# Optimization experiments

Measured on AMD Instinct MI355X. Metric: run time of the kernel, lower is better.

The kernel has to match this reference:

```python
import jax, jax.numpy as jnp
import numpy as np

N_HEADS = 16


def sparsemax(z):
    """Sparsemax along the last axis (Martins & Astudillo 2016)."""
    S = z.shape[-1]
    z_sorted = -jnp.sort(-z, axis=-1)                      # descending
    cs = jnp.cumsum(z_sorted, axis=-1)
    k = jnp.arange(1, S + 1, dtype=z.dtype)
    support = (1.0 + k * z_sorted) > cs                    # bool mask of support
    k_z = jnp.sum(support.astype(jnp.int32), axis=-1, keepdims=True)  # support size >=1
    cs_k = jnp.take_along_axis(cs, k_z - 1, axis=-1)
    tau = (cs_k - 1.0) / k_z.astype(z.dtype)
    return jnp.maximum(z - tau, 0.0)


def setup_inputs() -> dict:
    key = jax.random.key(0)
    ks = jax.random.split(key, 5)
    B, S, D = 4, 1024, 1024
    scale = 1.0 / np.sqrt(D).astype(np.float32)
    return {
        "x": jax.random.normal(ks[0], (B, S, D), jnp.float32),
        "Wq": jax.random.normal(ks[1], (D, D), jnp.float32) * scale,
        "bq": jnp.zeros((D,), jnp.float32),
        "Wk": jax.random.normal(ks[2], (D, D), jnp.float32) * scale,
        "bk": jnp.zeros((D,), jnp.float32),
        "Wv": jax.random.normal(ks[3], (D, D), jnp.float32) * scale,
        "bv": jnp.zeros((D,), jnp.float32),
        "Wo": jax.random.normal(ks[4], (D, D), jnp.float32) * scale,
        "bo": jnp.zeros((D,), jnp.float32),
    }


def reference(x, Wq, bq, Wk, bk, Wv, bv, Wo, bo):
    B, S, D = x.shape
    H = N_HEADS
    dh = D // H
    q = x @ Wq + bq                                        # (B,S,D)
    k = x @ Wk + bk
    v = x @ Wv + bv
    # split to heads: (B,H,S,dh)
    qh = q.reshape(B, S, H, dh).transpose(0, 2, 1, 3)
    kh = k.reshape(B, S, H, dh).transpose(0, 2, 1, 3)
    logits = jnp.einsum("bhqd,bhkd->bhqk", qh, kh) / np.sqrt(dh).astype(np.float32)
    probs = sparsemax(logits)                              # (B,H,S,S)
    # shared V: mean over head components, replicated per head
    v_shared = v.reshape(B, S, H, dh).mean(axis=2)         # (B,S,dh)
    out_h = jnp.einsum("bhqk,bkd->bhqd", probs, v_shared)  # (B,H,S,dh)
    x_out = out_h.transpose(0, 2, 1, 3).reshape(B, S, D) @ Wo + bo
    avg_attention = probs.mean(axis=1)                     # (B,S,S)
    return (x_out, avg_attention)
```

## Files before the change

kernel.cpp:

```cpp
#include <hip/hip_runtime.h>

#define B_  4
#define S_  1024
#define D_  1024
#define H_  16
#define DH  64
#define BS  4096

typedef __bf16 bf16x8 __attribute__((ext_vector_type(8)));
typedef float  f32x4  __attribute__((ext_vector_type(4)));

__device__ __forceinline__ unsigned short f2bf(float f) {
    __bf16 b = (__bf16)f;
    return __builtin_bit_cast(unsigned short, b);
}
__device__ __forceinline__ float bf2f(unsigned short u) {
    return (float)__builtin_bit_cast(__bf16, u);
}
__device__ __forceinline__ void glds16(const void* g, void* l) {
    __builtin_amdgcn_global_load_lds((const __attribute__((address_space(1))) void*)g,
                                     (__attribute__((address_space(3))) void*)l, 16, 0, 0);
}

__global__ __launch_bounds__(256) void prep2(const float* __restrict__ Wq,
                                             const float* __restrict__ Wk,
                                             const float* __restrict__ Wo,
                                             const float* __restrict__ Wv,
                                             const float* __restrict__ bv,
                                             unsigned short* __restrict__ WqTh,
                                             unsigned short* __restrict__ WqTl,
                                             unsigned short* __restrict__ WkTh,
                                             unsigned short* __restrict__ WkTl,
                                             unsigned short* __restrict__ WoTh,
                                             unsigned short* __restrict__ WvTh,
                                             unsigned short* __restrict__ WvTl,
                                             float* __restrict__ bvp) {
    __shared__ float tile[32][33];
    int bid = blockIdx.x, tid = threadIdx.x;
    if (bid < 3072) {
        const float* W;
        unsigned short *Th, *Tl;
        int wantLo;
        if (bid < 1024)      { W = Wq; Th = WqTh; Tl = WqTl; wantLo = 1; }
        else if (bid < 2048) { W = Wk; Th = WkTh; Tl = WkTl; wantLo = 1; bid -= 1024; }
        else                 { W = Wo; Th = WoTh; Tl = nullptr; wantLo = 0; bid -= 2048; }
        int tn = bid & 31, tk = bid >> 5;
        int r = tid >> 3, c4 = (tid & 7) * 4;
        float4 v = *(const float4*)(W + (size_t)(tk * 32 + r) * D_ + tn * 32 + c4);
        tile[r][c4 + 0] = v.x;
        tile[r][c4 + 1] = v.y;
        tile[r][c4 + 2] = v.z;
        tile[r][c4 + 3] = v.w;
        __syncthreads();
        unsigned short hh[4], ll[4];
#pragma unroll
        for (int i = 0; i < 4; i++) {
            float f = tile[c4 + i][r];
            hh[i] = f2bf(f);
            ll[i] = f2bf(f - bf2f(hh[i]));
        }
        size_t off = (size_t)(tn * 32 + r) * D_ + tk * 32 + c4;
        *(uint2*)(Th + off) = make_uint2((unsigned)hh[0] | ((unsigned)hh[1] << 16),
                                         (unsigned)hh[2] | ((unsigned)hh[3] << 16));
        if (wantLo)
            *(uint2*)(Tl + off) = make_uint2((unsigned)ll[0] | ((unsigned)ll[1] << 16),
                                             (unsigned)ll[2] | ((unsigned)ll[3] << 16));
    } else if (bid < 3328) {
        int e = (bid - 3072) * 256 + tid;
        int d = e >> 6, j = e & 63;
        float s = 0.f;
#pragma unroll
        for (int hh = 0; hh < H_; hh++) s += Wv[(size_t)d * D_ + hh * DH + j];
        s *= (1.f / 16.f);
        unsigned short hi = f2bf(s);
        WvTh[(size_t)j * D_ + d] = hi;
        WvTl[(size_t)j * D_ + d] = f2bf(s - bf2f(hi));
        if (bid == 3072 && tid < 128) {
            float sb = 0.f;
            if (tid < 64) {
#pragma unroll
                for (int hh = 0; hh < H_; hh++) sb += bv[hh * DH + tid];
                sb *= (1.f / 16.f);
            }
            bvp[tid] = sb;
        }
    } else {
        int e = (bid - 3328) * 256 + tid;
        int row = 64 + (e >> 10), col = e & 1023;
        WvTh[(size_t)row * D_ + col] = 0;
        WvTl[(size_t)row * D_ + col] = 0;
    }
}

__global__ __launch_bounds__(256) void projg(const float* __restrict__ x,
                                             const unsigned short* __restrict__ WqTh, const unsigned short* __restrict__ WqTl,
                                             const unsigned short* __restrict__ WkTh, const unsigned short* __restrict__ WkTl,
                                             const unsigned short* __restrict__ WvTh, const unsigned short* __restrict__ WvTl,
                                             const float* __restrict__ bq, const float* __restrict__ bk,
                                             const float* __restrict__ bvp,
                                             unsigned short* __restrict__ qh, unsigned short* __restrict__ ql,
                                             unsigned short* __restrict__ kh, unsigned short* __restrict__ kl,
                                             float* __restrict__ vshb) {
    __shared__ unsigned short AhS[128 * 32];
    __shared__ unsigned short AlS[128 * 32];
    __shared__ unsigned short BhS[128 * 32];
    __shared__ unsigned short BlS[128 * 32];

    int tid = threadIdx.x, w = tid >> 6, lane = tid & 63;
    int m16 = lane & 15, qd = lane >> 4;
    int bn = blockIdx.x, bm = blockIdx.y;

    const unsigned short *Bh, *Bl;
    const float* bias;
    int mode;
    if (bn < 8)       { Bh = WqTh + (size_t)bn * 128 * D_;       Bl = WqTl + (size_t)bn * 128 * D_;       bias = bq + bn * 128;       mode = 0; }
    else if (bn < 16) { Bh = WkTh + (size_t)(bn - 8) * 128 * D_; Bl = WkTl + (size_t)(bn - 8) * 128 * D_; bias = bk + (bn - 8) * 128; mode = 1; }
    else              { Bh = WvTh; Bl = WvTl; bias = bvp; mode = 2; }

    int l4 = lane >> 2, c8 = (lane & 3) * 8;
    int rh = (w >> 1) * 64, chh = (w & 1) * 64;

    f32x4 acc[4][4];
#pragma unroll
    for (int it = 0; it < 4; it++)
#pragma unroll
        for (int jt = 0; jt < 4; jt++) acc[it][jt] = (f32x4){0.f, 0.f, 0.f, 0.f};

    int ra = tid >> 1, ca = (tid & 1) * 16;

    for (int k0 = 0; k0 < D_; k0 += 32) {
        const float* ax = x + (size_t)(bm * 128 + ra) * D_ + k0 + ca;
        float4 f0 = *(const float4*)(ax + 0);
        float4 f1 = *(const float4*)(ax + 4);
        float4 f2 = *(const float4*)(ax + 8);
        float4 f3 = *(const float4*)(ax + 12);
        __syncthreads();
        {
            float vv[16] = {f0.x, f0.y, f0.z, f0.w, f1.x, f1.y, f1.z, f1.w,
                            f2.x, f2.y, f2.z, f2.w, f3.x, f3.y, f3.z, f3.w};
            unsigned int hw[8], lw[8];
#pragma unroll
            for (int i = 0; i < 8; i++) {
                unsigned short h0 = f2bf(vv[2 * i]), h1 = f2bf(vv[2 * i + 1]);
                unsigned short l0 = f2bf(vv[2 * i] - bf2f(h0));
                unsigned short l1 = f2bf(vv[2 * i + 1] - bf2f(h1));
                hw[i] = (unsigned)h0 | ((unsigned)h1 << 16);
                lw[i] = (unsigned)l0 | ((unsigned)l1 << 16);
            }
            char* ah = (char*)AhS + ra * 64 + ca * 2;
            char* al = (char*)AlS + ra * 64 + ca * 2;
            *(uint4*)(ah + 0)  = make_uint4(hw[0], hw[1], hw[2], hw[3]);
            *(uint4*)(ah + 16) = make_uint4(hw[4], hw[5], hw[6], hw[7]);
            *(uint4*)(al + 0)  = make_uint4(lw[0], lw[1], lw[2], lw[3]);
            *(uint4*)(al + 16) = make_uint4(lw[4], lw[5], lw[6], lw[7]);
        }
        {
            const unsigned short* gbh = Bh + (size_t)(w * 32 + l4) * D_ + k0 + c8;
            const unsigned short* gbl = Bl + (size_t)(w * 32 + l4) * D_ + k0 + c8;
            glds16(gbh,                     (char*)BhS + w * 2048);
            glds16(gbh + (size_t)16 * D_,   (char*)BhS + w * 2048 + 1024);
            glds16(gbl,                     (char*)BlS + w * 2048);
            glds16(gbl + (size_t)16 * D_,   (char*)BlS + w * 2048 + 1024);
        }
        __syncthreads();
        bf16x8 ah[4], al[4], bh[4], bl[4];
#pragma unroll
        for (int it = 0; it < 4; it++) {
            ah[it] = *(const bf16x8*)((char*)AhS + (rh + it * 16 + m16) * 64 + qd * 16);
            al[it] = *(const bf16x8*)((char*)AlS + (rh + it * 16 + m16) * 64 + qd * 16);
        }
#pragma unroll
        for (int jt = 0; jt < 4; jt++) {
            bh[jt] = *(const bf16x8*)((char*)BhS + (chh + jt * 16 + m16) * 64 + qd * 16);
            bl[jt] = *(const bf16x8*)((char*)BlS + (chh + jt * 16 + m16) * 64 + qd * 16);
        }
#pragma unroll
        for (int it = 0; it < 4; it++)
#pragma unroll
            for (int jt = 0; jt < 4; jt++) {
                acc[it][jt] = __builtin_amdgcn_mfma_f32_16x16x32_bf16(ah[it], bh[jt], acc[it][jt], 0, 0, 0);
                acc[it][jt] = __builtin_amdgcn_mfma_f32_16x16x32_bf16(ah[it], bl[jt], acc[it][jt], 0, 0, 0);
                acc[it][jt] = __builtin_amdgcn_mfma_f32_16x16x32_bf16(al[it], bh[jt], acc[it][jt], 0, 0, 0);
            }
    }
#pragma unroll
    for (int it = 0; it < 4; it++)
#pragma unroll
        for (int jt = 0; jt < 4; jt++)
#pragma unroll
            for (int r = 0; r < 4; r++) {
                int R = bm * 128 + rh + it * 16 + qd * 4 + r;
                int c = chh + jt * 16 + m16;
                float v = acc[it][jt][r] + bias[c];
                if (mode == 0) {
                    v *= 0.125f;
                    unsigned short h0 = f2bf(v);
                    qh[(size_t)R * D_ + bn * 128 + c] = h0;
                    ql[(size_t)R * D_ + bn * 128 + c] = f2bf(v - bf2f(h0));
                } else if (mode == 1) {
                    unsigned short h0 = f2bf(v);
                    kh[(size_t)R * D_ + (bn - 8) * 128 + c] = h0;
                    kl[(size_t)R * D_ + (bn - 8) * 128 + c] = f2bf(v - bf2f(h0));
                } else {
                    if (c < 64) vshb[(size_t)R * 64 + c] = v;
                }
            }
}

__global__ __launch_bounds__(256) void outg(const unsigned short* __restrict__ A,
                                            const unsigned short* __restrict__ Bh,
                                            const float* __restrict__ bias,
                                            float* __restrict__ C) {
    __shared__ unsigned short AhS[128 * 32];
    __shared__ unsigned short BhS[128 * 32];

    int tid = threadIdx.x, w = tid >> 6, lane = tid & 63;
    int m16 = lane & 15, qd = lane >> 4;
    int bn = blockIdx.x, bm = blockIdx.y;
    int l4 = lane >> 2, c8 = (lane & 3) * 8;
    int rh = (w >> 1) * 64, chh = (w & 1) * 64;

    f32x4 acc[4][4];
#pragma unroll
    for (int it = 0; it < 4; it++)
#pragma unroll
        for (int jt = 0; jt < 4; jt++) acc[it][jt] = (f32x4){0.f, 0.f, 0.f, 0.f};

    for (int k0 = 0; k0 < D_; k0 += 32) {
        __syncthreads();
        {
            const unsigned short* ga = A + (size_t)(bm * 128 + w * 32 + l4) * D_ + k0 + c8;
            glds16(ga,                   (char*)AhS + w * 2048);
            glds16(ga + (size_t)16 * D_, (char*)AhS + w * 2048 + 1024);
            const unsigned short* gb = Bh + (size_t)(bn * 128 + w * 32 + l4) * D_ + k0 + c8;
            glds16(gb,                   (char*)BhS + w * 2048);
            glds16(gb + (size_t)16 * D_, (char*)BhS + w * 2048 + 1024);
        }
        __syncthreads();
        bf16x8 ah[4], bh[4];
#pragma unroll
        for (int it = 0; it < 4; it++)
            ah[it] = *(const bf16x8*)((char*)AhS + (rh + it * 16 + m16) * 64 + qd * 16);
#pragma unroll
        for (int jt = 0; jt < 4; jt++)
            bh[jt] = *(const bf16x8*)((char*)BhS + (chh + jt * 16 + m16) * 64 + qd * 16);
#pragma unroll
        for (int it = 0; it < 4; it++)
#pragma unroll
            for (int jt = 0; jt < 4; jt++)
                acc[it][jt] = __builtin_amdgcn_mfma_f32_16x16x32_bf16(ah[it], bh[jt], acc[it][jt], 0, 0, 0);
    }
#pragma unroll
    for (int it = 0; it < 4; it++)
#pragma unroll
        for (int jt = 0; jt < 4; jt++)
#pragma unroll
            for (int r = 0; r < 4; r++) {
                int R = bm * 128 + rh + it * 16 + qd * 4 + r;
                int cc = bn * 128 + chh + jt * 16 + m16;
                C[(size_t)R * D_ + cc] = acc[it][jt][r] + bias[cc];
            }
}

#define CCAP 48
__global__ __launch_bounds__(256, 2) void attn8(const unsigned short* __restrict__ qh,
                                                const unsigned short* __restrict__ ql,
                                                const unsigned short* __restrict__ kh,
                                                const unsigned short* __restrict__ kl,
                                                const float* __restrict__ vsh,
                                                unsigned short* __restrict__ och,
                                                unsigned short* __restrict__ sidx,
                                                unsigned short* __restrict__ sval,
                                                int* __restrict__ scnt) {
    __shared__ float smM[4][16];
    __shared__ float smS[4][16], smC[4][16];
    __shared__ float tau0s[16];
    __shared__ float taus[16];
    __shared__ float candV[16][CCAP];
    __shared__ short candI[16][CCAP];
    __shared__ int   ccnt[16];
    __shared__ int   ovfAny;
    __shared__ int   scnt16[16];
    __shared__ short slotI[16][16];
    __shared__ float slotV[16][16];

    int tid = threadIdx.x, w = tid >> 6, lane = tid & 63;
    int m16 = lane & 15, qd = lane >> 4;

    int bid = blockIdx.x;
    int xcd = bid & 7;
    int j   = bid >> 3;
    int bh  = ((j & 7) << 3) | xcd;
    int qt  = j >> 3;
    int bb  = bh >> 4, h = bh & 15;
    int row0g = bb * S_ + qt * 16;
    int kbase = bb * S_;

    bf16x8 aH[2], aL[2];
#pragma unroll
    for (int c = 0; c < 2; c++) {
        size_t off = (size_t)(row0g + m16) * D_ + h * DH + c * 32 + qd * 8;
        aH[c] = *(const bf16x8*)(qh + off);
        aL[c] = *(const bf16x8*)(ql + off);
    }

    f32x4 Cfr[16];
#pragma unroll
    for (int t = 0; t < 16; t++) Cfr[t] = (f32x4){0.f, 0.f, 0.f, 0.f};

#pragma unroll
    for (int tb = 0; tb < 4; tb++) {
        bf16x8 bH[4][2], bL[4][2];
#pragma unroll
        for (int tt = 0; tt < 4; tt++) {
            int n0 = w * 256 + (tb * 4 + tt) * 16;
#pragma unroll
            for (int c = 0; c < 2; c++) {
                size_t boff = (size_t)(kbase + n0 + m16) * D_ + h * DH + c * 32 + qd * 8;
                bH[tt][c] = *(const bf16x8*)(kh + boff);
                bL[tt][c] = *(const bf16x8*)(kl + boff);
            }
        }
#pragma unroll
        for (int tt = 0; tt < 4; tt++) {
            int t = tb * 4 + tt;
            f32x4 a = Cfr[t];
            a = __builtin_amdgcn_mfma_f32_16x16x32_bf16(aH[0], bH[tt][0], a, 0, 0, 0);
            a = __builtin_amdgcn_mfma_f32_16x16x32_bf16(aH[1], bH[tt][1], a, 0, 0, 0);
            a = __builtin_amdgcn_mfma_f32_16x16x32_bf16(aH[0], bL[tt][0], a, 0, 0, 0);
            a = __builtin_amdgcn_mfma_f32_16x16x32_bf16(aH[1], bL[tt][1], a, 0, 0, 0);
            a = __builtin_amdgcn_mfma_f32_16x16x32_bf16(aL[0], bH[tt][0], a, 0, 0, 0);
            a = __builtin_amdgcn_mfma_f32_16x16x32_bf16(aL[1], bH[tt][1], a, 0, 0, 0);
            Cfr[t] = a;
        }
    }

    float mxr[4];
#pragma unroll
    for (int r = 0; r < 4; r++) mxr[r] = -3.0e38f;
#pragma unroll
    for (int t = 0; t < 16; t++)
#pragma unroll
        for (int r = 0; r < 4; r++) mxr[r] = fmaxf(mxr[r], Cfr[t][r]);
#pragma unroll
    for (int off = 8; off >= 1; off >>= 1)
#pragma unroll
        for (int r = 0; r < 4; r++) mxr[r] = fmaxf(mxr[r], __shfl_xor(mxr[r], off, 16));
    if (m16 == 0)
#pragma unroll
        for (int r = 0; r < 4; r++) smM[w][qd * 4 + r] = mxr[r];
    if (tid < 16) ccnt[tid] = 0;
    if (tid == 0) ovfAny = 0;
    __syncthreads();
    if (tid < 16)
        tau0s[tid] = fmaxf(fmaxf(smM[0][tid], smM[1][tid]), fmaxf(smM[2][tid], smM[3][tid])) - 1.0f;
    __syncthreads();

#pragma unroll
    for (int t = 0; t < 16; t++)
#pragma unroll
        for (int r = 0; r < 4; r++) {
            float z = Cfr[t][r];
            int row = qd * 4 + r;
            if (z > tau0s[row]) {
                int pos = atomicAdd(&ccnt[row], 1);
                if (pos < CCAP) {
                    candV[row][pos] = z;
                    candI[row][pos] = (short)(w * 256 + t * 16 + m16);
                }
            }
        }
    __syncthreads();
    if (tid < 16 && ccnt[tid] > CCAP) ovfAny = 1;

    int prow = tid >> 4, pc = tid & 15;
    int nc = ccnt[prow];
    float tau = tau0s[prow];
    float z0 = -3.0e38f, z1 = -3.0e38f, z2 = -3.0e38f;
    if (nc <= CCAP) {
        z0 = (pc < nc)      ? candV[prow][pc]      : -3.0e38f;
        z1 = (pc + 16 < nc) ? candV[prow][pc + 16] : -3.0e38f;
        z2 = (pc + 32 < nc) ? candV[prow][pc + 32] : -3.0e38f;
        for (int it = 0; it < CCAP; it++) {
            float s = 0.f, c = 0.f;
            if (z0 > tau) { s += z0; c += 1.f; }
            if (z1 > tau) { s += z1; c += 1.f; }
            if (z2 > tau) { s += z2; c += 1.f; }
#pragma unroll
            for (int off = 8; off >= 1; off >>= 1) {
                s += __shfl_xor(s, off, 16);
                c += __shfl_xor(c, off, 16);
            }
            float tnew = (s - 1.f) / c;
            if (tnew > tau) tau = tnew; else break;
        }
    }
    if (pc == 0) taus[prow] = tau;
    if (tid < 16) scnt16[tid] = 0;
    __syncthreads();

    if (!ovfAny) {
        if (z0 > tau) {
            int sl = atomicAdd(&scnt16[prow], 1);
            if (sl < 16) { slotI[prow][sl] = candI[prow][pc]; slotV[prow][sl] = z0 - tau; }
        }
        if (z1 > tau) {
            int sl = atomicAdd(&scnt16[prow], 1);
            if (sl < 16) { slotI[prow][sl] = candI[prow][pc + 16]; slotV[prow][sl] = z1 - tau; }
        }
        if (z2 > tau) {
            int sl = atomicAdd(&scnt16[prow], 1);
            if (sl < 16) { slotI[prow][sl] = candI[prow][pc + 32]; slotV[prow][sl] = z2 - tau; }
        }
        __syncthreads();
    } else {
        for (int it = 0; it < 64; it++) {
            float s[4], c[4];
#pragma unroll
            for (int r = 0; r < 4; r++) { s[r] = 0.f; c[r] = 0.f; }
#pragma unroll
            for (int t = 0; t < 16; t++)
#pragma unroll
                for (int r = 0; r < 4; r++) {
                    float z = Cfr[t][r];
                    if (z > taus[qd * 4 + r]) { s[r] += z; c[r] += 1.f; }
                }
#pragma unroll
            for (int off = 8; off >= 1; off >>= 1)
#pragma unroll
                for (int r = 0; r < 4; r++) {
                    s[r] += __shfl_xor(s[r], off, 16);
                    c[r] += __shfl_xor(c[r], off, 16);
                }
            if (m16 == 0)
#pragma unroll
                for (int r = 0; r < 4; r++) {
                    smS[w][qd * 4 + r] = s[r];
                    smC[w][qd * 4 + r] = c[r];
                }
            __syncthreads();
            int done = 1;
            if (tid < 16) {
                float S = smS[0][tid] + smS[1][tid] + smS[2][tid] + smS[3][tid];
                float C = smC[0][tid] + smC[1][tid] + smC[2][tid] + smC[3][tid];
                float tnew = (S - 1.f) / C;
                if (C > 0.f && tnew > taus[tid]) { taus[tid] = tnew; done = 0; }
            }
            if (__syncthreads_and(done)) break;
        }
#pragma unroll
        for (int t = 0; t < 16; t++)
#pragma unroll
            for (int r = 0; r < 4; r++) {
                int row = qd * 4 + r;
                float p = Cfr[t][r] - taus[row];
                if (p > 0.f) {
                    int sl = atomicAdd(&scnt16[row], 1);
                    if (sl < 16) {
                        slotI[row][sl] = (short)(w * 256 + t * 16 + m16);
                        slotV[row][sl] = p;
                    }
                }
            }
        __syncthreads();
    }

    int nsl = min(scnt16[prow], 16);
    float4 accq = make_float4(0.f, 0.f, 0.f, 0.f);
    for (int sl = 0; sl < nsl; sl++) {
        int key = slotI[prow][sl];
        float p = slotV[prow][sl];
        float4 vv = *(const float4*)(vsh + (size_t)(kbase + key) * DH + pc * 4);
        accq.x += p * vv.x;
        accq.y += p * vv.y;
        accq.z += p * vv.z;
        accq.w += p * vv.w;
    }
    {
        unsigned short b0 = f2bf(accq.x), b1 = f2bf(accq.y), b2 = f2bf(accq.z), b3 = f2bf(accq.w);
        *(uint2*)(och + (size_t)(row0g + prow) * D_ + h * DH + pc * 4) =
            make_uint2((unsigned)b0 | ((unsigned)b1 << 16), (unsigned)b2 | ((unsigned)b3 << 16));
    }
    {
        size_t base = ((size_t)(row0g + prow) * H_ + h) * 16;
        if (pc == 0) scnt[(row0g + prow) * H_ + h] = nsl;
        if (pc < nsl) {
            sidx[base + pc] = (unsigned short)slotI[prow][pc];
            sval[base + pc] = f2bf(slotV[prow][pc]);
        }
    }
}

__global__ __launch_bounds__(256) void avg_reduce(const unsigned short* __restrict__ sidx,
                                                  const unsigned short* __restrict__ sval,
                                                  const int* __restrict__ scnt,
                                                  float* __restrict__ avg) {
    __shared__ float accv[1024];
    int tid = threadIdx.x;
    int grow = blockIdx.x;
    for (int i = tid; i < 1024; i += 256) accv[i] = 0.f;
    __syncthreads();
    int h = tid >> 4, sl = tid & 15;
    int n = scnt[grow * H_ + h];
    if (sl < n) {
        size_t base = ((size_t)grow * H_ + h) * 16;
        int idx = sidx[base + sl];
        float v = bf2f(sval[base + sl]);
        atomicAdd(&accv[idx], v);
    }
    __syncthreads();
    float* dst = avg + (size_t)grow * S_;
    for (int i = tid; i < 256; i += 256) {
        float4 o;
        o.x = accv[i * 4 + 0] * 0.0625f;
        o.y = accv[i * 4 + 1] * 0.0625f;
        o.z = accv[i * 4 + 2] * 0.0625f;
        o.w = accv[i * 4 + 3] * 0.0625f;
        *(float4*)(dst + i * 4) = o;
    }
}

extern "C" void kernel_launch(void* const* d_in, const int* in_sizes, int n_in,
                              void* d_out, int out_size, void* d_ws, size_t ws_size,
                              hipStream_t stream) {
    const float* x  = (const float*)d_in[0];
    const float* Wq = (const float*)d_in[1];
    const float* bq = (const float*)d_in[2];
    const float* Wk = (const float*)d_in[3];
    const float* bk = (const float*)d_in[4];
    const float* Wv = (const float*)d_in[5];
    const float* bv = (const float*)d_in[6];
    const float* Wo = (const float*)d_in[7];
    const float* bo = (const float*)d_in[8];

    float* xout = (float*)d_out;
    float* avg  = xout + (size_t)BS * D_;

    char* ws = (char*)d_ws;
    unsigned short* qhB  = (unsigned short*)(ws + 0);
    unsigned short* qlB  = (unsigned short*)(ws + (8u << 20));
    unsigned short* khB  = (unsigned short*)(ws + (16u << 20));
    unsigned short* klB  = (unsigned short*)(ws + (24u << 20));
    unsigned short* WqTh = (unsigned short*)(ws + (32u << 20));
    unsigned short* WqTl = (unsigned short*)(ws + (34u << 20));
    unsigned short* WkTh = (unsigned short*)(ws + (36u << 20));
    unsigned short* WkTl = (unsigned short*)(ws + (38u << 20));
    unsigned short* ochB = WqTh;
    unsigned short* WoTh = (unsigned short*)(ws + (40u << 20));
    unsigned short* WvTh = (unsigned short*)(ws + (42u << 20));
    unsigned short* WvTl = (unsigned short*)(ws + (42u << 20) + (256u << 10));
    float* bvp = (float*)(ws + (42u << 20) + (512u << 10));
    float* vshb = (float*)(ws + (43u << 20));
    unsigned short* sidx = (unsigned short*)(ws + (44u << 20));
    unsigned short* sval = (unsigned short*)(ws + (46u << 20));
    int* scnt = (int*)(ws + (48u << 20));

    prep2<<<3584, 256, 0, stream>>>(Wq, Wk, Wo, Wv, bv, WqTh, WqTl, WkTh, WkTl, WoTh, WvTh, WvTl, bvp);
    projg<<<dim3(17, 32), 256, 0, stream>>>(x, WqTh, WqTl, WkTh, WkTl, WvTh, WvTl,
                                            bq, bk, bvp, qhB, qlB, khB, klB, vshb);
    attn8<<<4096, 256, 0, stream>>>(qhB, qlB, khB, klB, vshb, ochB, sidx, sval, scnt);
    avg_reduce<<<4096, 256, 0, stream>>>(sidx, sval, scnt, avg);
    outg<<<dim3(8, 32), 256, 0, stream>>>(ochB, WoTh, bo, xout);
}
```

Before: 399.1 us.

## Stage K tiles through swizzled LDS with double-buffered async loads in attn8

```diff
diff --git a/kernel.cpp b/kernel.cpp
--- a/kernel.cpp
+++ b/kernel.cpp
@@ -263,7 +263,7 @@
 }
 
 #define CCAP 48
-__global__ __launch_bounds__(256, 2) void attn8(const unsigned short* __restrict__ qh,
+__global__ __launch_bounds__(256, 4) void attn8(const unsigned short* __restrict__ qh,
                                                 const unsigned short* __restrict__ ql,
                                                 const unsigned short* __restrict__ kh,
                                                 const unsigned short* __restrict__ kl,
@@ -272,17 +272,19 @@
                                                 unsigned short* __restrict__ sidx,
                                                 unsigned short* __restrict__ sval,
                                                 int* __restrict__ scnt) {
+    __shared__ __align__(16) char KST[32768];
     __shared__ float smM[4][16];
     __shared__ float smS[4][16], smC[4][16];
     __shared__ float tau0s[16];
     __shared__ float taus[16];
-    __shared__ float candV[16][CCAP];
-    __shared__ short candI[16][CCAP];
     __shared__ int   ccnt[16];
     __shared__ int   ovfAny;
     __shared__ int   scnt16[16];
-    __shared__ short slotI[16][16];
-    __shared__ float slotV[16][16];
+
+    float (*candV)[CCAP] = (float (*)[CCAP])(KST);
+    short (*candI)[CCAP] = (short (*)[CCAP])(KST + 3072);
+    float (*slotV)[16]   = (float (*)[16])(KST + 4608);
+    short (*slotI)[16]   = (short (*)[16])(KST + 5632);
 
     int tid = threadIdx.x, w = tid >> 6, lane = tid & 63;
     int m16 = lane & 15, qd = lane >> 4;
@@ -308,31 +310,53 @@
 #pragma unroll
     for (int t = 0; t < 16; t++) Cfr[t] = (f32x4){0.f, 0.f, 0.f, 0.f};
 
-#pragma unroll
-    for (int tb = 0; tb < 4; tb++) {
-        bf16x8 bH[4][2], bL[4][2];
-#pragma unroll
-        for (int tt = 0; tt < 4; tt++) {
-            int n0 = w * 256 + (tb * 4 + tt) * 16;
-#pragma unroll
-            for (int c = 0; c < 2; c++) {
-                size_t boff = (size_t)(kbase + n0 + m16) * D_ + h * DH + c * 32 + qd * 8;
-                bH[tt][c] = *(const bf16x8*)(kh + boff);
-                bL[tt][c] = *(const bf16x8*)(kl + boff);
-            }
-        }
-#pragma unroll
-        for (int tt = 0; tt < 4; tt++) {
-            int t = tb * 4 + tt;
+    char* myK = KST + w * 8192;
+    {
+        int sr = lane >> 3;
+        int sc = (lane & 7) ^ sr;
+        const unsigned short* ksh = kh + (size_t)(kbase + w * 256 + sr) * D_ + h * DH + sc * 8;
+        const unsigned short* ksl = kl + (size_t)(kbase + w * 256 + sr) * D_ + h * DH + sc * 8;
+
+#define STAGE_K(t, buf) do {                                        \
+        size_t o_ = (size_t)(t) * 16 * D_;                          \
+        char* db_ = myK + (buf) * 4096;                             \
+        glds16(ksh + o_,                  db_);                     \
+        glds16(ksh + o_ + (size_t)8 * D_, db_ + 1024);              \
+        glds16(ksl + o_,                  db_ + 2048);              \
+        glds16(ksl + o_ + (size_t)8 * D_, db_ + 3072);              \
+    } while (0)
+
+        int sw0 = m16 * 128 + (((qd    ) ^ (m16 & 7)) << 4);
+        int sw1 = m16 * 128 + (((4 + qd) ^ (m16 & 7)) << 4);
+
+        STAGE_K(0, 0);
+        asm volatile("s_waitcnt vmcnt(0)" ::: "memory");
+        __builtin_amdgcn_sched_barrier(0);
+
+#pragma unroll
+        for (int t = 0; t < 16; t++) {
+            if (t < 15) {
+                STAGE_K(t + 1, (t + 1) & 1);
+                asm volatile("s_waitcnt vmcnt(4)" ::: "memory");
+            } else {
+                asm volatile("s_waitcnt vmcnt(0)" ::: "memory");
+            }
+            __builtin_amdgcn_sched_barrier(0);
+            const char* tbuf = myK + (t & 1) * 4096;
+            bf16x8 bfh0 = *(const bf16x8*)(tbuf + sw0);
+            bf16x8 bfh1 = *(const bf16x8*)(tbuf + sw1);
+            bf16x8 bfl0 = *(const bf16x8*)(tbuf + 2048 + sw0);
+            bf16x8 bfl1 = *(const bf16x8*)(tbuf + 2048 + sw1);
             f32x4 a = Cfr[t];
-            a = __builtin_amdgcn_mfma_f32_16x16x32_bf16(aH[0], bH[tt][0], a, 0, 0, 0);
-            a = __builtin_amdgcn_mfma_f32_16x16x32_bf16(aH[1], bH[tt][1], a, 0, 0, 0);
-            a = __builtin_amdgcn_mfma_f32_16x16x32_bf16(aH[0], bL[tt][0], a, 0, 0, 0);
-            a = __builtin_amdgcn_mfma_f32_16x16x32_bf16(aH[1], bL[tt][1], a, 0, 0, 0);
-            a = __builtin_amdgcn_mfma_f32_16x16x32_bf16(aL[0], bH[tt][0], a, 0, 0, 0);
-            a = __builtin_amdgcn_mfma_f32_16x16x32_bf16(aL[1], bH[tt][1], a, 0, 0, 0);
+            a = __builtin_amdgcn_mfma_f32_16x16x32_bf16(aH[0], bfh0, a, 0, 0, 0);
+            a = __builtin_amdgcn_mfma_f32_16x16x32_bf16(aH[1], bfh1, a, 0, 0, 0);
+            a = __builtin_amdgcn_mfma_f32_16x16x32_bf16(aH[0], bfl0, a, 0, 0, 0);
+            a = __builtin_amdgcn_mfma_f32_16x16x32_bf16(aH[1], bfl1, a, 0, 0, 0);
+            a = __builtin_amdgcn_mfma_f32_16x16x32_bf16(aL[0], bfh0, a, 0, 0, 0);
+            a = __builtin_amdgcn_mfma_f32_16x16x32_bf16(aL[1], bfh1, a, 0, 0, 0);
             Cfr[t] = a;
         }
+#undef STAGE_K
     }
 
     float mxr[4];
```

Result: faster. 363.0 us (-9.0%).
